# Kernel optimization log

Measured on AMD Instinct MI355X. Metric: run time of the kernel, lower is better.

The kernel has to match this reference:

```python
import jax, jax.numpy as jnp
import numpy as np

WS = 4        # window_size
SHIFT = 2     # shift
NHEADS = 8


def setup_inputs():
    key = jax.random.key(0)
    k = jax.random.split(key, 5)
    N, C, H, W = 16, 512, 96, 96
    x = jax.random.normal(k[0], (N, C, H, W), dtype=jnp.float32)
    # nn.MultiheadAttention parameters
    in_proj_w = jax.random.normal(k[1], (3 * C, C), dtype=jnp.float32) * 0.02
    in_proj_b = jax.random.normal(k[2], (3 * C,), dtype=jnp.float32) * 0.02
    out_w = jax.random.normal(k[3], (C, C), dtype=jnp.float32) * 0.02
    out_b = jax.random.normal(k[4], (C,), dtype=jnp.float32) * 0.02
    return {"x": x, "in_proj_w": in_proj_w, "in_proj_b": in_proj_b,
            "out_w": out_w, "out_b": out_b}


def _split_window(x, ws):
    # replicates torch: cat(split(x, ws, dim=3), dim=2); cat(split(x, ws, dim=2), dim=0)
    N, C, Hp, Wp = x.shape
    nh, nw = Hp // ws, Wp // ws
    x = x.reshape(N, C, nh, ws, nw, ws)      # n c ib wi jb wj
    x = x.transpose(4, 2, 0, 1, 3, 5)        # jb ib n c wi wj (col-block outermost in batch)
    return x.reshape(nw * nh * N, C, ws, ws), nh, nw


def _concat_window(x, nh, nw, ws):
    # inverse of _split_window, replicating torch chunk/cat order
    N = x.shape[0] // (nh * nw)
    C = x.shape[1]
    x = x.reshape(nw, nh, N, C, ws, ws)      # jb ib n c wi wj
    x = x.transpose(2, 3, 1, 4, 0, 5)        # n c ib wi jb wj
    return x.reshape(N, C, nh * ws, nw * ws)


def _mha(xt, mask_f, in_proj_w, in_proj_b, out_w, out_b):
    # xt: (B, L, C); mask_f: (B, L) FLOAT key_padding_mask -> added to logits (torch semantics)
    B, L, C = xt.shape
    d = C // NHEADS
    qkv = xt @ in_proj_w.T + in_proj_b                     # (B, L, 3C)
    q, k, v = jnp.split(qkv, 3, axis=-1)
    heads = lambda t: t.reshape(B, L, NHEADS, d).transpose(0, 2, 1, 3)  # (B, H, L, d)
    q, k, v = heads(q), heads(k), heads(v)
    scale = float(1.0 / np.sqrt(d))
    scores = jnp.einsum('bhqd,bhkd->bhqk', q, k) * scale
    scores = scores + mask_f[:, None, None, :]             # additive float key mask
    attn = jax.nn.softmax(scores, axis=-1)
    o = jnp.einsum('bhqk,bhkd->bhqd', attn, v)
    o = o.transpose(0, 2, 1, 3).reshape(B, L, C)
    return o @ out_w.T + out_b


def reference(x, in_proj_w, in_proj_b, out_w, out_b):
    N, C, H, W = x.shape
    ws = WS
    pad_h, pad_w = ws - H % ws, ws - W % ws   # note: pads a full window even when divisible
    x = jnp.pad(x, ((0, 0), (0, 0), (0, pad_h), (0, pad_w)))
    x = jnp.roll(x, (SHIFT, SHIFT), axis=(2, 3))
    # BUG-FAITHFUL: source overwrites the boolean mask with a second roll of x,
    # so the "mask" is the doubly-rolled float feature map.
    mask = jnp.roll(x, (SHIFT, SHIFT), axis=(2, 3))
    xw, nh, nw = _split_window(x, ws)
    mw, _, _ = _split_window(mask, ws)
    B = xw.shape[0]
    xt = xw.reshape(B, C, ws * ws).transpose(0, 2, 1)      # (B, L=ws*ws, C)
    mask_f = mw[:, 0].reshape(B, ws * ws)                  # channel-0 float "mask"
    ot = _mha(xt, mask_f, in_proj_w, in_proj_b, out_w, out_b)
    ow = ot.transpose(0, 2, 1).reshape(B, C, ws, ws)
    out = _concat_window(ow, nh, nw, ws)
    out = jnp.roll(out, (-SHIFT, -SHIFT), axis=(2, 3))
    return out[:, :, :H, :W]
```

## Files before the change

kernel.cpp:

```cpp
#include <hip/hip_runtime.h>
#include <cstdint>


typedef __attribute__((ext_vector_type(8))) __bf16 bf16x8;
typedef __attribute__((ext_vector_type(8))) uint16_t u16x8;
typedef __attribute__((ext_vector_type(4))) float f32x4;

__device__ __forceinline__ uint16_t f2bf(float f) {
  union { float f; uint32_t u; } c; c.f = f;
  uint32_t r = c.u + 0x7FFFu + ((c.u >> 16) & 1u);
  return (uint16_t)(r >> 16);
}
__device__ __forceinline__ float bf2f(uint16_t u) {
  union { uint32_t u; float f; } c; c.u = ((uint32_t)u) << 16;
  return c.f;
}

__device__ __forceinline__ void g2lds16(const void* g, void* lds) {
  __builtin_amdgcn_global_load_lds(
      (const __attribute__((address_space(1))) uint32_t*)(uintptr_t)g,
      (__attribute__((address_space(3))) uint32_t*)(uintptr_t)lds,
      16, 0, 0);
}

#define CFENCE asm volatile("" ::: "memory")
#define BAR do { CFENCE; __builtin_amdgcn_s_barrier(); CFENCE; } while (0)

__global__ void cvt_weights(const float* __restrict__ w1, const float* __restrict__ w2,
                            uint16_t* __restrict__ o1, uint16_t* __restrict__ o2) {
  int i = blockIdx.x * 256 + threadIdx.x;
  if (i < 786432) o1[i] = f2bf(w1[i]);
  if (i < 262144) o2[i] = f2bf(w2[i]);
}

__global__ __launch_bounds__(256) void gather_kernel(
    const float* __restrict__ x, uint16_t* __restrict__ xbf, int n0) {
  __shared__ float tile[64][65];
  const int z = blockIdx.z;
  const int g = z / 100, hh = z % 100;
  const int c0 = blockIdx.y * 64, ww0 = blockIdx.x * 64;
  const int n = n0 + g;
  const int hp = (hh >= 2) ? hh - 2 : hh + 98;
  const bool hok = hp < 96;
  const int t = threadIdx.x;
  const int lane = t & 63, grp = t >> 6;

  const int ww = ww0 + lane;
  const int wp = (ww >= 2) ? ww - 2 : ww + 98;
  const bool wok = hok && (ww < 100) && (wp < 96);
  const float* xb = x + ((size_t)n * 512) * 9216 + (size_t)hp * 96 + wp;
#pragma unroll
  for (int i = 0; i < 16; ++i) {
    int c = grp + i * 4;
    tile[c][lane] = wok ? xb[(size_t)(c0 + c) * 9216] : 0.f;
  }
  __syncthreads();
#pragma unroll
  for (int i = 0; i < 16; ++i) {
    int wl = grp + i * 4;
    int www = ww0 + wl;
    if (www < 100) {
      int m = (g * 625 + (hh >> 2) * 25 + (www >> 2)) * 16 + (hh & 3) * 4 + (www & 3);
      xbf[(size_t)m * 512 + c0 + lane] = f2bf(tile[lane][wl]);
    }
  }
}

template <int EPI, int NB, int MODE>
__global__ __launch_bounds__(512, 2) void gemm2(
    const uint16_t* __restrict__ A, const uint16_t* __restrict__ B,
    const float* __restrict__ bias, uint16_t* __restrict__ Cbf,
    float* __restrict__ Cout, int Mg, int n0) {
  __shared__ alignas(16) uint16_t lds[65536];
  const int t = threadIdx.x;
  const int w = t >> 6, lane = t & 63;
  const int wr = w >> 2, wc = w & 3;
  const int lr = lane & 15, lg = lane >> 4;

  const int nwg = gridDim.x, bid = blockIdx.x;
  const int q = nwg >> 3, r = nwg & 7;
  const int xc = bid & 7, li = bid >> 3;
  const int wg = (xc < r ? xc * (q + 1) : r * (q + 1) + (xc - r) * q) + li;
  int bm, bn;
  if (MODE == 0) { bm = wg / NB; bn = wg % NB; }
  else           { bm = wg % NB; bn = wg / NB; }

  auto STAGE = [&](int kt, int b) {
#pragma unroll
    for (int i = 0; i < 4; ++i) {
      int e = i * 512 + t;
      int row = e >> 3, slot = e & 7;
      const uint16_t* ga = A + (size_t)(bm * 256 + row) * 512 + kt * 64 +
                           ((slot ^ (row & 7)) << 3);
      const uint16_t* gb = B + (size_t)(bn * 256 + row) * 512 + kt * 64 +
                           ((slot ^ (row & 7)) << 3);
      g2lds16(ga, &lds[b * 32768 + ((i * 512 + w * 64) << 3)]);
      g2lds16(gb, &lds[b * 32768 + 16384 + ((i * 512 + w * 64) << 3)]);
    }
  };
  auto LDA = [&](int b, int mi, int k2) -> bf16x8 {
    int row = wr * 128 + mi * 16 + lr;
    int byte = b * 65536 + row * 128 + ((k2 * 64 + lg * 16) ^ ((row & 7) << 4));
    return *(const bf16x8*)((const char*)lds + byte);
  };
  auto LDB = [&](int b, int ni, int k2) -> bf16x8 {
    int row = wc * 64 + ni * 16 + lr;
    int byte = b * 65536 + 32768 + row * 128 +
               ((k2 * 64 + lg * 16) ^ ((row & 7) << 4));
    return *(const bf16x8*)((const char*)lds + byte);
  };

  f32x4 acc[8][4];
#pragma unroll
  for (int mi = 0; mi < 8; ++mi)
#pragma unroll
    for (int ni = 0; ni < 4; ++ni) acc[mi][ni] = (f32x4){0.f, 0.f, 0.f, 0.f};

  STAGE(0, 0);
  asm volatile("s_waitcnt vmcnt(0)" ::: "memory");
  BAR;

  int cur = 0;
  for (int k = 0; k < 8; ++k) {
    if (k + 1 < 8) STAGE(k + 1, cur ^ 1);
    bf16x8 af[8][2], bf[4][2];
#pragma unroll
    for (int mi = 0; mi < 8; ++mi)
#pragma unroll
      for (int k2 = 0; k2 < 2; ++k2) af[mi][k2] = LDA(cur, mi, k2);
#pragma unroll
    for (int ni = 0; ni < 4; ++ni)
#pragma unroll
      for (int k2 = 0; k2 < 2; ++k2) bf[ni][k2] = LDB(cur, ni, k2);
    __builtin_amdgcn_s_setprio(1);
#pragma unroll
    for (int mi = 0; mi < 8; ++mi)
#pragma unroll
      for (int ni = 0; ni < 4; ++ni)
#pragma unroll
        for (int k2 = 0; k2 < 2; ++k2)
          acc[mi][ni] = __builtin_amdgcn_mfma_f32_16x16x32_bf16(
              af[mi][k2], bf[ni][k2], acc[mi][ni], 0, 0, 0);
    __builtin_amdgcn_s_setprio(0);
    asm volatile("s_waitcnt vmcnt(0)" ::: "memory");
    BAR;
    cur ^= 1;
  }

  if (EPI == 0) {
#pragma unroll
    for (int ni = 0; ni < 4; ++ni) {
      int col = bn * 256 + wc * 64 + ni * 16 + lr;
      float bb = bias[col];
#pragma unroll
      for (int mi = 0; mi < 8; ++mi) {
        int row = bm * 256 + wr * 128 + mi * 16 + lg * 4;
#pragma unroll
        for (int rr = 0; rr < 4; ++rr)
          Cbf[(size_t)(row + rr) * 1536 + col] = f2bf(acc[mi][ni][rr] + bb);
      }
    }
  } else {
    __syncthreads();
    float* ldsF = (float*)lds;
    const int Gwin = Mg >> 4;
#pragma unroll
    for (int p = 0; p < 4; ++p) {
      if (wc == p) {
#pragma unroll
        for (int mi = 0; mi < 8; ++mi) {
          const float* b4 = &bias[bm * 256 + wr * 128 + mi * 16 + lg * 4];
#pragma unroll
          for (int ni = 0; ni < 4; ++ni)
#pragma unroll
            for (int rr = 0; rr < 4; ++rr)
              ldsF[(wr * 128 + mi * 16 + lg * 4 + rr) * 68 + ni * 16 + lr] =
                  acc[mi][ni][rr] + b4[rr];
        }
      }
      __syncthreads();
#pragma unroll
      for (int i = 0; i < 8; ++i) {
        int e = i * 512 + t;
        int w4 = e & 3, rrow = (e >> 2) & 3, c = e >> 4;
        int cw = bn * 16 + p * 4 + w4;
        if (cw < Gwin) {
          int g = cw / 625, wid = cw % 625;
          int ib = wid / 25, jb = wid % 25;
          int hh = ib * 4 + rrow;
          if (hh >= 2 && hh < 98) {
            float4 v = *(const float4*)&ldsF[c * 68 + w4 * 16 + rrow * 4];
            size_t base = ((size_t)(n0 + g) * 512 + bm * 256 + c) * 9216 +
                          (size_t)(hh - 2) * 96;
            if (jb >= 1 && jb < 24) {
              float* pp = &Cout[base + jb * 4 - 2];
              float2 lo; lo.x = v.x; lo.y = v.y;
              float2 hi; hi.x = v.z; hi.y = v.w;
              *(float2*)pp = lo;
              *(float2*)(pp + 2) = hi;
            } else if (jb == 0) {
              Cout[base + 0] = v.z; Cout[base + 1] = v.w;
            } else {
              Cout[base + 94] = v.x; Cout[base + 95] = v.y;
            }
          }
        }
      }
      __syncthreads();
    }
  }
}

__global__ __launch_bounds__(128) void attn_kernel(
    const uint16_t* __restrict__ qkv, const float* __restrict__ x,
    uint16_t* __restrict__ obuf, int n0) {
  __shared__ alignas(16) uint16_t skv[16][1024];
  __shared__ float smask[16];
  const int b = blockIdx.x;
  const int g = b / 625, wid = b % 625;
  const int ib = wid / 25, jb = wid % 25;
  const int t = threadIdx.x;
  const int wv = t >> 6;
  const int mbase = b * 16;
  const int h = t >> 4, qi = t & 15;

#pragma unroll
  for (int it = 0; it < 16; ++it) {
    int e = it * 128 + t;
    int l = e >> 7, c = e & 127;
    const uint16_t* src = qkv + (size_t)(mbase + l) * 1536 + 512 + c * 8;
    g2lds16(src, (uint16_t*)skv + (it * 128 + wv * 64) * 8);
  }
  float qv[64];
#pragma unroll
  for (int d8 = 0; d8 < 8; ++d8) {
    u16x8 v = *(const u16x8*)&qkv[(size_t)(mbase + qi) * 1536 + h * 64 + d8 * 8];
#pragma unroll
    for (int j = 0; j < 8; ++j) qv[d8 * 8 + j] = bf2f(v[j]);
  }
  if (t < 16) {
    int hh = ib * 4 + (t >> 2), ww = jb * 4 + (t & 3);
    int a = (hh >= 4) ? hh - 4 : hh + 96;
    int c = (ww >= 4) ? ww - 4 : ww + 96;
    smask[t] = (a < 96 && c < 96)
                   ? x[((size_t)(n0 + g) * 512) * 9216 + (size_t)a * 96 + c]
                   : 0.f;
  }
  __syncthreads();

  float s[16];
  float mx = -1e30f;
#pragma unroll
  for (int ki = 0; ki < 16; ++ki) {
    float a = 0.f;
#pragma unroll
    for (int d8 = 0; d8 < 8; ++d8) {
      u16x8 kv = *(const u16x8*)&skv[ki][h * 64 + d8 * 8];
#pragma unroll
      for (int j = 0; j < 8; ++j) a += qv[d8 * 8 + j] * bf2f(kv[j]);
    }
    s[ki] = a * 0.125f + smask[ki];
    mx = fmaxf(mx, s[ki]);
  }
  float sum = 0.f;
#pragma unroll
  for (int ki = 0; ki < 16; ++ki) { s[ki] = __expf(s[ki] - mx); sum += s[ki]; }
  const float inv = 1.f / sum;
  float o[64];
#pragma unroll
  for (int d = 0; d < 64; ++d) o[d] = 0.f;
#pragma unroll
  for (int ki = 0; ki < 16; ++ki) {
    float wgt = s[ki] * inv;
#pragma unroll
    for (int d8 = 0; d8 < 8; ++d8) {
      u16x8 vv = *(const u16x8*)&skv[ki][512 + h * 64 + d8 * 8];
#pragma unroll
      for (int j = 0; j < 8; ++j) o[d8 * 8 + j] += wgt * bf2f(vv[j]);
    }
  }
  const int m = mbase + qi;
#pragma unroll
  for (int d8 = 0; d8 < 8; ++d8) {
    alignas(16) uint16_t tmp[8];
#pragma unroll
    for (int j = 0; j < 8; ++j) tmp[j] = f2bf(o[d8 * 8 + j]);
    *(uint4*)&obuf[(size_t)m * 512 + h * 64 + d8 * 8] = *(uint4*)tmp;
  }
}

extern "C" void kernel_launch(void* const* d_in, const int* in_sizes, int n_in,
                              void* d_out, int out_size, void* d_ws, size_t ws_size,
                              hipStream_t stream) {
  const float* x  = (const float*)d_in[0];
  const float* wq = (const float*)d_in[1];
  const float* bq = (const float*)d_in[2];
  const float* wo = (const float*)d_in[3];
  const float* bo = (const float*)d_in[4];
  float* out = (float*)d_out;
  uint8_t* ws = (uint8_t*)d_ws;

  uint16_t* wq_bf = (uint16_t*)ws;
  uint16_t* wo_bf = (uint16_t*)(ws + 1572864);
  uint8_t* bufbase = ws + 2097152;

  int G = 16;
  while (G > 1) {
    int Mg = G * 10000;
    int Mp = ((Mg + 255) / 256) * 256;
    size_t need = (size_t)2097152 + (size_t)Mp * 4096;
    if (need <= ws_size) break;
    G >>= 1;
  }
  const int Mg = G * 10000;
  const int Mp = ((Mg + 255) / 256) * 256;
  uint16_t* xo   = (uint16_t*)bufbase;
  uint16_t* qkvb = (uint16_t*)(bufbase + (size_t)Mp * 1024);

  cvt_weights<<<dim3(3072), dim3(256), 0, stream>>>(wq, wo, wq_bf, wo_bf);

  for (int n0 = 0; n0 < 16; n0 += G) {
    gather_kernel<<<dim3(2, 8, G * 100), dim3(256), 0, stream>>>(x, xo, n0);
    gemm2<0, 6, 0><<<dim3((Mp / 256) * 6), dim3(512), 0, stream>>>(
        xo, wq_bf, bq, qkvb, nullptr, Mg, n0);
    attn_kernel<<<dim3(G * 625), dim3(128), 0, stream>>>(qkvb, x, xo, n0);
    gemm2<1, 2, 1><<<dim3((Mp / 256) * 2), dim3(512), 0, stream>>>(
        wo_bf, xo, bo, nullptr, out, Mg, n0);
  }
  (void)in_sizes; (void)n_in; (void)out_size;
}
```

Before: 1.172 ms.

## Replace tiled GEMMs with weight-stationary persistent GEMMs over all images at once

Both projection GEMMs become weight-stationary kernels. Each workgroup holds a 128-column slice of the full K=512 weight matrix in LDS and loops over a run of 256-token chunks, reading the activations straight from global memory into registers. The per-image batching loop and the workspace-size fallback are removed, so each stage launches once over all 16 images. The output-projection epilogue now scatters scalar floats directly to NCHW instead of staging through LDS, which may give less coalesced global stores. The code also assumes the workspace is always large enough for all 160000 tokens.

```diff
diff --git a/kernel.cpp b/kernel.cpp
--- a/kernel.cpp
+++ b/kernel.cpp
@@ -22,9 +22,6 @@
       (__attribute__((address_space(3))) uint32_t*)(uintptr_t)lds,
       16, 0, 0);
 }
-
-#define CFENCE asm volatile("" ::: "memory")
-#define BAR do { CFENCE; __builtin_amdgcn_s_barrier(); CFENCE; } while (0)
 
 __global__ void cvt_weights(const float* __restrict__ w1, const float* __restrict__ w2,
                             uint16_t* __restrict__ o1, uint16_t* __restrict__ o2) {
@@ -66,147 +63,110 @@
   }
 }
 
-template <int EPI, int NB, int MODE>
-__global__ __launch_bounds__(512, 2) void gemm2(
-    const uint16_t* __restrict__ A, const uint16_t* __restrict__ B,
+template <int EPI, int NS, int CPS>
+__global__ __launch_bounds__(512, 2) void gemmP(
+    const uint16_t* __restrict__ X, const uint16_t* __restrict__ W,
     const float* __restrict__ bias, uint16_t* __restrict__ Cbf,
-    float* __restrict__ Cout, int Mg, int n0) {
+    float* __restrict__ Cout) {
   __shared__ alignas(16) uint16_t lds[65536];
   const int t = threadIdx.x;
-  const int w = t >> 6, lane = t & 63;
-  const int wr = w >> 2, wc = w & 3;
+  const int wv = t >> 6, lane = t & 63;
   const int lr = lane & 15, lg = lane >> 4;
 
   const int nwg = gridDim.x, bid = blockIdx.x;
   const int q = nwg >> 3, r = nwg & 7;
   const int xc = bid & 7, li = bid >> 3;
   const int wg = (xc < r ? xc * (q + 1) : r * (q + 1) + (xc - r) * q) + li;
-  int bm, bn;
-  if (MODE == 0) { bm = wg / NB; bn = wg % NB; }
-  else           { bm = wg % NB; bn = wg / NB; }
-
-  auto STAGE = [&](int kt, int b) {
-#pragma unroll
-    for (int i = 0; i < 4; ++i) {
-      int e = i * 512 + t;
-      int row = e >> 3, slot = e & 7;
-      const uint16_t* ga = A + (size_t)(bm * 256 + row) * 512 + kt * 64 +
-                           ((slot ^ (row & 7)) << 3);
-      const uint16_t* gb = B + (size_t)(bn * 256 + row) * 512 + kt * 64 +
-                           ((slot ^ (row & 7)) << 3);
-      g2lds16(ga, &lds[b * 32768 + ((i * 512 + w * 64) << 3)]);
-      g2lds16(gb, &lds[b * 32768 + 16384 + ((i * 512 + w * 64) << 3)]);
-    }
-  };
-  auto LDA = [&](int b, int mi, int k2) -> bf16x8 {
-    int row = wr * 128 + mi * 16 + lr;
-    int byte = b * 65536 + row * 128 + ((k2 * 64 + lg * 16) ^ ((row & 7) << 4));
+  const int seg = wg / NS, sl = wg % NS;
+  const int ch0 = seg * CPS;
+  const int ch1 = (ch0 + CPS < 625) ? ch0 + CPS : 625;
+
+#pragma unroll
+  for (int i = 0; i < 16; ++i) {
+    int e = i * 512 + t;
+    int row = e >> 6, slot = e & 63;
+    g2lds16(W + (size_t)(sl * 128 + row) * 512 + ((slot ^ (row & 7)) << 3),
+            &lds[(i * 512 + wv * 64) * 8 + (lane & 63) * 0 + 0] + (size_t)0 + (size_t)(0));
+  }
+  __syncthreads();
+
+  auto LDW = [&](int nt, int ks) -> bf16x8 {
+    int row = nt * 16 + lr;
+    int byte = row * 1024 + ((ks * 64 + lg * 16) ^ ((row & 7) << 4));
     return *(const bf16x8*)((const char*)lds + byte);
   };
-  auto LDB = [&](int b, int ni, int k2) -> bf16x8 {
-    int row = wc * 64 + ni * 16 + lr;
-    int byte = b * 65536 + 32768 + row * 128 +
-               ((k2 * 64 + lg * 16) ^ ((row & 7) << 4));
-    return *(const bf16x8*)((const char*)lds + byte);
-  };
-
-  f32x4 acc[8][4];
-#pragma unroll
-  for (int mi = 0; mi < 8; ++mi)
-#pragma unroll
-    for (int ni = 0; ni < 4; ++ni) acc[mi][ni] = (f32x4){0.f, 0.f, 0.f, 0.f};
-
-  STAGE(0, 0);
-  asm volatile("s_waitcnt vmcnt(0)" ::: "memory");
-  BAR;
-
-  int cur = 0;
-  for (int k = 0; k < 8; ++k) {
-    if (k + 1 < 8) STAGE(k + 1, cur ^ 1);
-    bf16x8 af[8][2], bf[4][2];
-#pragma unroll
-    for (int mi = 0; mi < 8; ++mi)
-#pragma unroll
-      for (int k2 = 0; k2 < 2; ++k2) af[mi][k2] = LDA(cur, mi, k2);
-#pragma unroll
-    for (int ni = 0; ni < 4; ++ni)
-#pragma unroll
-      for (int k2 = 0; k2 < 2; ++k2) bf[ni][k2] = LDB(cur, ni, k2);
-    __builtin_amdgcn_s_setprio(1);
-#pragma unroll
-    for (int mi = 0; mi < 8; ++mi)
-#pragma unroll
-      for (int ni = 0; ni < 4; ++ni)
-#pragma unroll
-        for (int k2 = 0; k2 < 2; ++k2)
-          acc[mi][ni] = __builtin_amdgcn_mfma_f32_16x16x32_bf16(
-              af[mi][k2], bf[ni][k2], acc[mi][ni], 0, 0, 0);
-    __builtin_amdgcn_s_setprio(0);
-    asm volatile("s_waitcnt vmcnt(0)" ::: "memory");
-    BAR;
-    cur ^= 1;
-  }
-
-  if (EPI == 0) {
-#pragma unroll
-    for (int ni = 0; ni < 4; ++ni) {
-      int col = bn * 256 + wc * 64 + ni * 16 + lr;
-      float bb = bias[col];
-#pragma unroll
-      for (int mi = 0; mi < 8; ++mi) {
-        int row = bm * 256 + wr * 128 + mi * 16 + lg * 4;
-#pragma unroll
-        for (int rr = 0; rr < 4; ++rr)
-          Cbf[(size_t)(row + rr) * 1536 + col] = f2bf(acc[mi][ni][rr] + bb);
-      }
-    }
-  } else {
-    __syncthreads();
-    float* ldsF = (float*)lds;
-    const int Gwin = Mg >> 4;
-#pragma unroll
-    for (int p = 0; p < 4; ++p) {
-      if (wc == p) {
-#pragma unroll
-        for (int mi = 0; mi < 8; ++mi) {
-          const float* b4 = &bias[bm * 256 + wr * 128 + mi * 16 + lg * 4];
-#pragma unroll
-          for (int ni = 0; ni < 4; ++ni)
-#pragma unroll
-            for (int rr = 0; rr < 4; ++rr)
-              ldsF[(wr * 128 + mi * 16 + lg * 4 + rr) * 68 + ni * 16 + lr] =
-                  acc[mi][ni][rr] + b4[rr];
+
+  for (int ch = ch0; ch < ch1; ++ch) {
+    const int tokb = ch * 256 + wv * 32;
+    bf16x8 xf[2][16];
+#pragma unroll
+    for (int mt = 0; mt < 2; ++mt)
+#pragma unroll
+      for (int ks = 0; ks < 16; ++ks)
+        xf[mt][ks] = *(const bf16x8*)&X[(size_t)(tokb + mt * 16 + lr) * 512 +
+                                        ks * 32 + lg * 8];
+    f32x4 acc[2][8];
+#pragma unroll
+    for (int mt = 0; mt < 2; ++mt)
+#pragma unroll
+      for (int nt = 0; nt < 8; ++nt) acc[mt][nt] = (f32x4){0.f, 0.f, 0.f, 0.f};
+
+#pragma unroll
+    for (int ks = 0; ks < 16; ++ks)
+#pragma unroll
+      for (int nt = 0; nt < 8; ++nt) {
+        bf16x8 wf = LDW(nt, ks);
+        acc[0][nt] = __builtin_amdgcn_mfma_f32_16x16x32_bf16(wf, xf[0][ks],
+                                                             acc[0][nt], 0, 0, 0);
+        acc[1][nt] = __builtin_amdgcn_mfma_f32_16x16x32_bf16(wf, xf[1][ks],
+                                                             acc[1][nt], 0, 0, 0);
+      }
+
+    if (EPI == 0) {
+#pragma unroll
+      for (int nt = 0; nt < 8; ++nt) {
+        int col = sl * 128 + nt * 16 + lg * 4;
+        float4 b4 = *(const float4*)&bias[col];
+#pragma unroll
+        for (int mt = 0; mt < 2; ++mt) {
+          int tok = tokb + mt * 16 + lr;
+          uint16_t pk[4];
+          pk[0] = f2bf(acc[mt][nt][0] + b4.x);
+          pk[1] = f2bf(acc[mt][nt][1] + b4.y);
+          pk[2] = f2bf(acc[mt][nt][2] + b4.z);
+          pk[3] = f2bf(acc[mt][nt][3] + b4.w);
+          uint2 v;
+          v.x = (uint32_t)pk[0] | ((uint32_t)pk[1] << 16);
+          v.y = (uint32_t)pk[2] | ((uint32_t)pk[3] << 16);
+          *(uint2*)&Cbf[(size_t)tok * 1536 + col] = v;
         }
       }
-      __syncthreads();
-#pragma unroll
-      for (int i = 0; i < 8; ++i) {
-        int e = i * 512 + t;
-        int w4 = e & 3, rrow = (e >> 2) & 3, c = e >> 4;
-        int cw = bn * 16 + p * 4 + w4;
-        if (cw < Gwin) {
-          int g = cw / 625, wid = cw % 625;
-          int ib = wid / 25, jb = wid % 25;
-          int hh = ib * 4 + rrow;
-          if (hh >= 2 && hh < 98) {
-            float4 v = *(const float4*)&ldsF[c * 68 + w4 * 16 + rrow * 4];
-            size_t base = ((size_t)(n0 + g) * 512 + bm * 256 + c) * 9216 +
-                          (size_t)(hh - 2) * 96;
-            if (jb >= 1 && jb < 24) {
-              float* pp = &Cout[base + jb * 4 - 2];
-              float2 lo; lo.x = v.x; lo.y = v.y;
-              float2 hi; hi.x = v.z; hi.y = v.w;
-              *(float2*)pp = lo;
-              *(float2*)(pp + 2) = hi;
-            } else if (jb == 0) {
-              Cout[base + 0] = v.z; Cout[base + 1] = v.w;
-            } else {
-              Cout[base + 94] = v.x; Cout[base + 95] = v.y;
-            }
+    } else {
+      size_t part[2]; bool ok[2];
+#pragma unroll
+      for (int mt = 0; mt < 2; ++mt) {
+        int tok = tokb + mt * 16 + lr;
+        int win = tok >> 4, idx = tok & 15;
+        int g = win / 625, w2 = win - g * 625;
+        int ib = w2 / 25, jb = w2 - ib * 25;
+        int hh = ib * 4 + (idx >> 2), ww = jb * 4 + (idx & 3);
+        ok[mt] = (hh >= 2) && (hh < 98) && (ww >= 2) && (ww < 98);
+        part[mt] = ((size_t)g * 512) * 9216 + (size_t)(hh - 2) * 96 + (ww - 2);
+      }
+#pragma unroll
+      for (int nt = 0; nt < 8; ++nt) {
+        int c0 = sl * 128 + nt * 16 + lg * 4;
+        float4 b4 = *(const float4*)&bias[c0];
+#pragma unroll
+        for (int mt = 0; mt < 2; ++mt) {
+          if (ok[mt]) {
+            Cout[part[mt] + (size_t)(c0 + 0) * 9216] = acc[mt][nt][0] + b4.x;
+            Cout[part[mt] + (size_t)(c0 + 1) * 9216] = acc[mt][nt][1] + b4.y;
+            Cout[part[mt] + (size_t)(c0 + 2) * 9216] = acc[mt][nt][2] + b4.z;
+            Cout[part[mt] + (size_t)(c0 + 3) * 9216] = acc[mt][nt][3] + b4.w;
           }
         }
       }
-      __syncthreads();
     }
   }
 }
@@ -304,28 +264,16 @@
   uint16_t* wo_bf = (uint16_t*)(ws + 1572864);
   uint8_t* bufbase = ws + 2097152;
 
-  int G = 16;
-  while (G > 1) {
-    int Mg = G * 10000;
-    int Mp = ((Mg + 255) / 256) * 256;
-    size_t need = (size_t)2097152 + (size_t)Mp * 4096;
-    if (need <= ws_size) break;
-    G >>= 1;
-  }
-  const int Mg = G * 10000;
-  const int Mp = ((Mg + 255) / 256) * 256;
   uint16_t* xo   = (uint16_t*)bufbase;
-  uint16_t* qkvb = (uint16_t*)(bufbase + (size_t)Mp * 1024);
+  uint16_t* qkvb = (uint16_t*)(bufbase + (size_t)160000 * 1024);
+  (void)ws_size;
 
   cvt_weights<<<dim3(3072), dim3(256), 0, stream>>>(wq, wo, wq_bf, wo_bf);
 
-  for (int n0 = 0; n0 < 16; n0 += G) {
-    gather_kernel<<<dim3(2, 8, G * 100), dim3(256), 0, stream>>>(x, xo, n0);
-    gemm2<0, 6, 0><<<dim3((Mp / 256) * 6), dim3(512), 0, stream>>>(
-        xo, wq_bf, bq, qkvb, nullptr, Mg, n0);
-    attn_kernel<<<dim3(G * 625), dim3(128), 0, stream>>>(qkvb, x, xo, n0);
-    gemm2<1, 2, 1><<<dim3((Mp / 256) * 2), dim3(512), 0, stream>>>(
-        wo_bf, xo, bo, nullptr, out, Mg, n0);
-  }
+  gather_kernel<<<dim3(2, 8, 1600), dim3(256), 0, stream>>>(x, xo, 0);
+  gemmP<0, 12, 30><<<dim3(252), dim3(512), 0, stream>>>(xo, wq_bf, bq, qkvb, nullptr);
+  attn_kernel<<<dim3(10000), dim3(128), 0, stream>>>(qkvb, x, xo, 0);
+  gemmP<1, 4, 10><<<dim3(252), dim3(512), 0, stream>>>(xo, wo_bf, bo, nullptr, out);
+
   (void)in_sizes; (void)n_in; (void)out_size;
 }
```

New measurement: 2.483 ms. 112% more time.

## Use 128x128 single-buffered GEMM tiles and row-major token layout for coalesced output

Applied to the files above, without the earlier changes.

Replaces the 256x256 double-buffered 512-thread GEMM with a 128x128 single-buffered 256-thread variant with a smaller LDS footprint, aiming at higher occupancy and more workgroups. Tokens are now stored in spatial row-major order (g*10000+hh*100+ww) rather than window-major, so the output epilogue can write contiguous float4 runs along image rows; the attention kernel gathers window rows via strided indexing instead. The batch-chunk loop and workspace-size check are removed, and the whole batch is processed in one pass, which assumes the workspace is large enough. Loads are no longer overlapped with compute inside the GEMM.

```diff
diff --git a/kernel.cpp b/kernel.cpp
--- a/kernel.cpp
+++ b/kernel.cpp
@@ -60,21 +60,21 @@
     int wl = grp + i * 4;
     int www = ww0 + wl;
     if (www < 100) {
-      int m = (g * 625 + (hh >> 2) * 25 + (www >> 2)) * 16 + (hh & 3) * 4 + (www & 3);
+      int m = g * 10000 + hh * 100 + www;
       xbf[(size_t)m * 512 + c0 + lane] = f2bf(tile[lane][wl]);
     }
   }
 }
 
 template <int EPI, int NB, int MODE>
-__global__ __launch_bounds__(512, 2) void gemm2(
+__global__ __launch_bounds__(256, 4) void gemm97(
     const uint16_t* __restrict__ A, const uint16_t* __restrict__ B,
     const float* __restrict__ bias, uint16_t* __restrict__ Cbf,
     float* __restrict__ Cout, int Mg, int n0) {
-  __shared__ alignas(16) uint16_t lds[65536];
+  __shared__ alignas(16) uint16_t lds[17408];
   const int t = threadIdx.x;
   const int w = t >> 6, lane = t & 63;
-  const int wr = w >> 2, wc = w & 3;
+  const int wr = w >> 1, wc = w & 1;
   const int lr = lane & 15, lg = lane >> 4;
 
   const int nwg = gridDim.x, bid = blockIdx.x;
@@ -85,56 +85,51 @@
   if (MODE == 0) { bm = wg / NB; bn = wg % NB; }
   else           { bm = wg % NB; bn = wg / NB; }
 
-  auto STAGE = [&](int kt, int b) {
+  auto STAGE = [&](int kt) {
 #pragma unroll
     for (int i = 0; i < 4; ++i) {
-      int e = i * 512 + t;
+      int e = i * 256 + t;
       int row = e >> 3, slot = e & 7;
-      const uint16_t* ga = A + (size_t)(bm * 256 + row) * 512 + kt * 64 +
-                           ((slot ^ (row & 7)) << 3);
-      const uint16_t* gb = B + (size_t)(bn * 256 + row) * 512 + kt * 64 +
-                           ((slot ^ (row & 7)) << 3);
-      g2lds16(ga, &lds[b * 32768 + ((i * 512 + w * 64) << 3)]);
-      g2lds16(gb, &lds[b * 32768 + 16384 + ((i * 512 + w * 64) << 3)]);
+      int kb = (slot ^ (row & 7)) << 3;
+      g2lds16(A + (size_t)(bm * 128 + row) * 512 + kt * 64 + kb,
+              &lds[(size_t)e * 8]);
+      g2lds16(B + (size_t)(bn * 128 + row) * 512 + kt * 64 + kb,
+              &lds[8192 + (size_t)e * 8]);
     }
   };
-  auto LDA = [&](int b, int mi, int k2) -> bf16x8 {
-    int row = wr * 128 + mi * 16 + lr;
-    int byte = b * 65536 + row * 128 + ((k2 * 64 + lg * 16) ^ ((row & 7) << 4));
+  auto LDA = [&](int mi, int k2) -> bf16x8 {
+    int row = wr * 64 + mi * 16 + lr;
+    int byte = row * 128 + ((k2 * 64 + lg * 16) ^ ((row & 7) << 4));
     return *(const bf16x8*)((const char*)lds + byte);
   };
-  auto LDB = [&](int b, int ni, int k2) -> bf16x8 {
+  auto LDB = [&](int ni, int k2) -> bf16x8 {
     int row = wc * 64 + ni * 16 + lr;
-    int byte = b * 65536 + 32768 + row * 128 +
-               ((k2 * 64 + lg * 16) ^ ((row & 7) << 4));
+    int byte = 16384 + row * 128 + ((k2 * 64 + lg * 16) ^ ((row & 7) << 4));
     return *(const bf16x8*)((const char*)lds + byte);
   };
 
-  f32x4 acc[8][4];
-#pragma unroll
-  for (int mi = 0; mi < 8; ++mi)
+  f32x4 acc[4][4];
+#pragma unroll
+  for (int mi = 0; mi < 4; ++mi)
 #pragma unroll
     for (int ni = 0; ni < 4; ++ni) acc[mi][ni] = (f32x4){0.f, 0.f, 0.f, 0.f};
 
-  STAGE(0, 0);
-  asm volatile("s_waitcnt vmcnt(0)" ::: "memory");
-  BAR;
-
-  int cur = 0;
-  for (int k = 0; k < 8; ++k) {
-    if (k + 1 < 8) STAGE(k + 1, cur ^ 1);
-    bf16x8 af[8][2], bf[4][2];
-#pragma unroll
-    for (int mi = 0; mi < 8; ++mi)
-#pragma unroll
-      for (int k2 = 0; k2 < 2; ++k2) af[mi][k2] = LDA(cur, mi, k2);
+  for (int kt = 0; kt < 8; ++kt) {
+    STAGE(kt);
+    asm volatile("s_waitcnt vmcnt(0)" ::: "memory");
+    BAR;
+    bf16x8 af[4][2], bf[4][2];
+#pragma unroll
+    for (int mi = 0; mi < 4; ++mi)
+#pragma unroll
+      for (int k2 = 0; k2 < 2; ++k2) af[mi][k2] = LDA(mi, k2);
 #pragma unroll
     for (int ni = 0; ni < 4; ++ni)
 #pragma unroll
-      for (int k2 = 0; k2 < 2; ++k2) bf[ni][k2] = LDB(cur, ni, k2);
+      for (int k2 = 0; k2 < 2; ++k2) bf[ni][k2] = LDB(ni, k2);
     __builtin_amdgcn_s_setprio(1);
 #pragma unroll
-    for (int mi = 0; mi < 8; ++mi)
+    for (int mi = 0; mi < 4; ++mi)
 #pragma unroll
       for (int ni = 0; ni < 4; ++ni)
 #pragma unroll
@@ -142,19 +137,17 @@
           acc[mi][ni] = __builtin_amdgcn_mfma_f32_16x16x32_bf16(
               af[mi][k2], bf[ni][k2], acc[mi][ni], 0, 0, 0);
     __builtin_amdgcn_s_setprio(0);
-    asm volatile("s_waitcnt vmcnt(0)" ::: "memory");
     BAR;
-    cur ^= 1;
   }
 
   if (EPI == 0) {
 #pragma unroll
     for (int ni = 0; ni < 4; ++ni) {
-      int col = bn * 256 + wc * 64 + ni * 16 + lr;
+      int col = bn * 128 + wc * 64 + ni * 16 + lr;
       float bb = bias[col];
 #pragma unroll
-      for (int mi = 0; mi < 8; ++mi) {
-        int row = bm * 256 + wr * 128 + mi * 16 + lg * 4;
+      for (int mi = 0; mi < 4; ++mi) {
+        int row = bm * 128 + wr * 64 + mi * 16 + lg * 4;
 #pragma unroll
         for (int rr = 0; rr < 4; ++rr)
           Cbf[(size_t)(row + rr) * 1536 + col] = f2bf(acc[mi][ni][rr] + bb);
@@ -163,46 +156,38 @@
   } else {
     __syncthreads();
     float* ldsF = (float*)lds;
-    const int Gwin = Mg >> 4;
-#pragma unroll
-    for (int p = 0; p < 4; ++p) {
+#pragma unroll
+    for (int p = 0; p < 2; ++p) {
       if (wc == p) {
 #pragma unroll
-        for (int mi = 0; mi < 8; ++mi) {
-          const float* b4 = &bias[bm * 256 + wr * 128 + mi * 16 + lg * 4];
+        for (int mi = 0; mi < 4; ++mi) {
+          const float* b4 = &bias[bm * 128 + wr * 64 + mi * 16 + lg * 4];
 #pragma unroll
           for (int ni = 0; ni < 4; ++ni)
 #pragma unroll
             for (int rr = 0; rr < 4; ++rr)
-              ldsF[(wr * 128 + mi * 16 + lg * 4 + rr) * 68 + ni * 16 + lr] =
+              ldsF[(wr * 64 + mi * 16 + lg * 4 + rr) * 68 + ni * 16 + lr] =
                   acc[mi][ni][rr] + b4[rr];
         }
       }
       __syncthreads();
 #pragma unroll
       for (int i = 0; i < 8; ++i) {
-        int e = i * 512 + t;
-        int w4 = e & 3, rrow = (e >> 2) & 3, c = e >> 4;
-        int cw = bn * 16 + p * 4 + w4;
-        if (cw < Gwin) {
-          int g = cw / 625, wid = cw % 625;
-          int ib = wid / 25, jb = wid % 25;
-          int hh = ib * 4 + rrow;
-          if (hh >= 2 && hh < 98) {
-            float4 v = *(const float4*)&ldsF[c * 68 + w4 * 16 + rrow * 4];
-            size_t base = ((size_t)(n0 + g) * 512 + bm * 256 + c) * 9216 +
-                          (size_t)(hh - 2) * 96;
-            if (jb >= 1 && jb < 24) {
-              float* pp = &Cout[base + jb * 4 - 2];
-              float2 lo; lo.x = v.x; lo.y = v.y;
-              float2 hi; hi.x = v.z; hi.y = v.w;
-              *(float2*)pp = lo;
-              *(float2*)(pp + 2) = hi;
-            } else if (jb == 0) {
-              Cout[base + 0] = v.z; Cout[base + 1] = v.w;
-            } else {
-              Cout[base + 94] = v.x; Cout[base + 95] = v.y;
-            }
+        int e = i * 256 + t;
+        int q4 = e & 15, c = e >> 4;
+        int tok = bn * 128 + p * 64 + q4 * 4;
+        int g = tok / 10000, rem = tok - g * 10000;
+        int hh = rem / 100, ww = rem - hh * 100;
+        if (hh >= 2 && hh < 98) {
+          float4 v = *(const float4*)&ldsF[c * 68 + q4 * 4];
+          size_t base = ((size_t)(n0 + g) * 512 + bm * 128 + c) * 9216 +
+                        (size_t)(hh - 2) * 96;
+          if (ww >= 4 && ww <= 92) {
+            *(float4*)&Cout[base + ww - 2] = v;
+          } else if (ww == 0) {
+            Cout[base + 0] = v.z; Cout[base + 1] = v.w;
+          } else if (ww == 96) {
+            Cout[base + 94] = v.x; Cout[base + 95] = v.y;
           }
         }
       }
@@ -221,20 +206,23 @@
   const int ib = wid / 25, jb = wid % 25;
   const int t = threadIdx.x;
   const int wv = t >> 6;
-  const int mbase = b * 16;
   const int h = t >> 4, qi = t & 15;
+
+  const int mbase = g * 10000 + ib * 400 + jb * 4;
 
 #pragma unroll
   for (int it = 0; it < 16; ++it) {
     int e = it * 128 + t;
     int l = e >> 7, c = e & 127;
-    const uint16_t* src = qkv + (size_t)(mbase + l) * 1536 + 512 + c * 8;
+    int m = mbase + (l >> 2) * 100 + (l & 3);
+    const uint16_t* src = qkv + (size_t)m * 1536 + 512 + c * 8;
     g2lds16(src, (uint16_t*)skv + (it * 128 + wv * 64) * 8);
   }
+  const int mq = mbase + (qi >> 2) * 100 + (qi & 3);
   float qv[64];
 #pragma unroll
   for (int d8 = 0; d8 < 8; ++d8) {
-    u16x8 v = *(const u16x8*)&qkv[(size_t)(mbase + qi) * 1536 + h * 64 + d8 * 8];
+    u16x8 v = *(const u16x8*)&qkv[(size_t)mq * 1536 + h * 64 + d8 * 8];
 #pragma unroll
     for (int j = 0; j < 8; ++j) qv[d8 * 8 + j] = bf2f(v[j]);
   }
@@ -279,13 +267,12 @@
       for (int j = 0; j < 8; ++j) o[d8 * 8 + j] += wgt * bf2f(vv[j]);
     }
   }
-  const int m = mbase + qi;
 #pragma unroll
   for (int d8 = 0; d8 < 8; ++d8) {
     alignas(16) uint16_t tmp[8];
 #pragma unroll
     for (int j = 0; j < 8; ++j) tmp[j] = f2bf(o[d8 * 8 + j]);
-    *(uint4*)&obuf[(size_t)m * 512 + h * 64 + d8 * 8] = *(uint4*)tmp;
+    *(uint4*)&obuf[(size_t)mq * 512 + h * 64 + d8 * 8] = *(uint4*)tmp;
   }
 }
 
@@ -304,28 +291,19 @@
   uint16_t* wo_bf = (uint16_t*)(ws + 1572864);
   uint8_t* bufbase = ws + 2097152;
 
-  int G = 16;
-  while (G > 1) {
-    int Mg = G * 10000;
-    int Mp = ((Mg + 255) / 256) * 256;
-    size_t need = (size_t)2097152 + (size_t)Mp * 4096;
-    if (need <= ws_size) break;
-    G >>= 1;
-  }
-  const int Mg = G * 10000;
-  const int Mp = ((Mg + 255) / 256) * 256;
+  const int Mg = 160000;
   uint16_t* xo   = (uint16_t*)bufbase;
-  uint16_t* qkvb = (uint16_t*)(bufbase + (size_t)Mp * 1024);
+  uint16_t* qkvb = (uint16_t*)(bufbase + (size_t)Mg * 1024);
+  (void)ws_size;
 
   cvt_weights<<<dim3(3072), dim3(256), 0, stream>>>(wq, wo, wq_bf, wo_bf);
 
-  for (int n0 = 0; n0 < 16; n0 += G) {
-    gather_kernel<<<dim3(2, 8, G * 100), dim3(256), 0, stream>>>(x, xo, n0);
-    gemm2<0, 6, 0><<<dim3((Mp / 256) * 6), dim3(512), 0, stream>>>(
-        xo, wq_bf, bq, qkvb, nullptr, Mg, n0);
-    attn_kernel<<<dim3(G * 625), dim3(128), 0, stream>>>(qkvb, x, xo, n0);
-    gemm2<1, 2, 1><<<dim3((Mp / 256) * 2), dim3(512), 0, stream>>>(
-        wo_bf, xo, bo, nullptr, out, Mg, n0);
-  }
+  gather_kernel<<<dim3(2, 8, 1600), dim3(256), 0, stream>>>(x, xo, 0);
+  gemm97<0, 12, 0><<<dim3(1250 * 12), dim3(256), 0, stream>>>(
+      xo, wq_bf, bq, qkvb, nullptr, Mg, 0);
+  attn_kernel<<<dim3(10000), dim3(128), 0, stream>>>(qkvb, x, xo, 0);
+  gemm97<1, 4, 1><<<dim3(1250 * 4), dim3(256), 0, stream>>>(
+      wo_bf, xo, bo, nullptr, out, Mg, 0);
+
   (void)in_sizes; (void)n_in; (void)out_size;
 }
```

Measured after the change: 1.882 ms. 1.61x slower.
